# Kernel optimization log

Measured on AMD Instinct MI355X. Metric: run time of the kernel, lower is better.

Reference implementation:

```python
import jax, jax.numpy as jnp
import numpy as np

B, T, D = 2, 2048, 1024
H = 16
DH = D // H


def setup_inputs() -> dict:
    key = jax.random.key(0)
    ks = jax.random.split(key, 6)
    s = 1.0 / np.sqrt(D)
    return {
        "x": jax.random.normal(ks[0], (B, T, D), dtype=jnp.float32),
        "Wq": jax.random.normal(ks[1], (D, D), dtype=jnp.float32) * s,
        "Wk": jax.random.normal(ks[2], (D, D), dtype=jnp.float32) * s,
        "Wv": jax.random.normal(ks[3], (D, D), dtype=jnp.float32) * s,
        "Wo": jax.random.normal(ks[4], (D, D), dtype=jnp.float32) * s,
        "bo": jax.random.normal(ks[5], (D,), dtype=jnp.float32) * s,
    }


def reference(x, Wq, Wk, Wv, Wo, bo):
    b, t, _ = x.shape
    # separate Q/K/V projections (nn.Linear: x @ W.T, no bias)
    q = (x @ Wq.T).reshape(b, t, H, DH).transpose(0, 2, 1, 3)  # [b,h,t,hd]
    k = (x @ Wk.T).reshape(b, t, H, DH).transpose(0, 2, 1, 3)
    v = (x @ Wv.T).reshape(b, t, H, DH).transpose(0, 2, 1, 3)

    scores = jnp.einsum("bhqd,bhkd->bhqk", q, k)  # [b,h,t,t]
    causal = jnp.triu(jnp.ones((t, t), dtype=bool), k=1)
    scores = jnp.where(causal, -jnp.inf, scores)
    weights = jax.nn.softmax(scores / np.sqrt(DH), axis=-1)
    # dropout p=0.0 -> identity
    ctx = jnp.einsum("bhqk,bhkd->bhqd", weights, v)  # [b,h,t,hd]
    # NOTE: original code reshapes WITHOUT transposing heads back — replicate faithfully
    ctx = ctx.reshape(b, t, H * DH)
    return ctx @ Wo.T + bo
```

## Files before the change

### kernel.cpp

```cpp
#include <hip/hip_runtime.h>
#include <math.h>

#define BATCH 2
#define SEQ   2048
#define DIM   1024
#define NH    16
#define HD    64
#define MTOT  4096

typedef __attribute__((ext_vector_type(8)))  short bf16x8;
typedef __attribute__((ext_vector_type(4)))  float f32x4;
typedef __attribute__((ext_vector_type(16))) float f32x16;
typedef __attribute__((ext_vector_type(2)))  float f32x2;
typedef __attribute__((ext_vector_type(2)))  unsigned u32x2;

__device__ __forceinline__ ushort f2bf(float f) {
    union { float f; unsigned u; } v; v.f = f;
    unsigned r = v.u + 0x7fffu + ((v.u >> 16) & 1u);
    return (ushort)(r >> 16);
}

__device__ __forceinline__ unsigned cvtpk_bf16(float lo, float hi) {
    unsigned r;
    asm("v_cvt_pk_bf16_f32 %0, %1, %2" : "=v"(r) : "v"(lo), "v"(hi));
    return r;
}

__device__ __forceinline__ f32x2 pk_add(f32x2 a, f32x2 b) {
    f32x2 d;
    asm("v_pk_add_f32 %0, %1, %2" : "=v"(d) : "v"(a), "v"(b));
    return d;
}

__device__ __forceinline__ f32x2 pk_mul(f32x2 a, f32x2 b) {
    f32x2 d;
    asm("v_pk_mul_f32 %0, %1, %2" : "=v"(d) : "v"(a), "v"(b));
    return d;
}

__device__ __forceinline__ float fmax3(float a, float b, float c) {
    return fmaxf(fmaxf(a, b), c);
}

__global__ __launch_bounds__(256)
void cast_all(const float* __restrict__ x,
              const float* __restrict__ Wq, const float* __restrict__ Wk,
              const float* __restrict__ Wv, const float* __restrict__ Wo,
              ushort* __restrict__ xb,
              ushort* __restrict__ wqb, ushort* __restrict__ wkb,
              ushort* __restrict__ wvb, ushort* __restrict__ wob)
{
    const int z = blockIdx.y;
    const float* s; ushort* d; int n4;
    if (z == 0)      { s = x;  d = xb;  n4 = MTOT * DIM / 4; }
    else if (z == 1) { s = Wq; d = wqb; n4 = DIM * DIM / 4; }
    else if (z == 2) { s = Wk; d = wkb; n4 = DIM * DIM / 4; }
    else if (z == 3) { s = Wv; d = wvb; n4 = DIM * DIM / 4; }
    else             { s = Wo; d = wob; n4 = DIM * DIM / 4; }
    for (int i = blockIdx.x * blockDim.x + threadIdx.x; i < n4;
         i += gridDim.x * blockDim.x) {
        float4 v = ((const float4*)s)[i];
        ushort4 o;
        o.x = f2bf(v.x); o.y = f2bf(v.y); o.z = f2bf(v.z); o.w = f2bf(v.w);
        ((ushort4*)d)[i] = o;
    }
}

template<int MODE>
__global__ __launch_bounds__(256)
void gemm_bf16(const ushort* __restrict__ A,
               const ushort* __restrict__ W0, const ushort* __restrict__ W1,
               const ushort* __restrict__ W2,
               ushort* __restrict__ D0, ushort* __restrict__ D1,
               ushort* __restrict__ D2,
               const float* __restrict__ bias, float* __restrict__ Fout)
{
    __shared__ __align__(16) ushort As[2][128 * 64];
    __shared__ __align__(16) ushort Bs[2][128 * 64];

    const int tid = threadIdx.x;
    const int w = tid >> 6, l = tid & 63;
    const int g = l >> 4, l15 = l & 15;
    const int wr = w >> 1, wc = w & 1;
    const int brow = blockIdx.x * 128, bcol = blockIdx.y * 128;

    const ushort* W = (MODE == 1) ? W0
                    : (blockIdx.z == 0 ? W0 : (blockIdx.z == 1 ? W1 : W2));
    ushort* Dst = (MODE == 1) ? (ushort*)0
                : (blockIdx.z == 0 ? D0 : (blockIdx.z == 1 ? D1 : D2));

    const int rsub = l >> 3;
    const int gc   = ((l & 7) ^ rsub) * 8;
    const size_t arow0 = (size_t)(brow + 32 * w + rsub) * DIM;
    const size_t brow0 = (size_t)(bcol + 32 * w + rsub) * DIM;

    auto STAGE = [&](int buf, int ktel) {
        #pragma unroll
        for (int i = 0; i < 4; ++i) {
            __builtin_amdgcn_global_load_lds(
                (const __attribute__((address_space(1))) void*)
                    &A[arow0 + (size_t)(8 * i) * DIM + ktel + gc],
                (__attribute__((address_space(3))) void*)
                    &As[buf][(32 * w + 8 * i) * 64], 16, 0, 0);
            __builtin_amdgcn_global_load_lds(
                (const __attribute__((address_space(1))) void*)
                    &W[brow0 + (size_t)(8 * i) * DIM + ktel + gc],
                (__attribute__((address_space(3))) void*)
                    &Bs[buf][(32 * w + 8 * i) * 64], 16, 0, 0);
        }
    };

    STAGE(0, 0);
    STAGE(1, 64);

    f32x4 acc[4][4] = {};

    for (int t = 0; t < 16; ++t) {
        const int cur = t & 1;
        if (t < 15) asm volatile("s_waitcnt vmcnt(8)" ::: "memory");
        else        asm volatile("s_waitcnt vmcnt(0)" ::: "memory");
        __builtin_amdgcn_s_barrier();
        __builtin_amdgcn_sched_barrier(0);

        #pragma unroll
        for (int kh = 0; kh < 2; ++kh) {
            bf16x8 af[4], bfr[4];
            #pragma unroll
            for (int mi = 0; mi < 4; ++mi) {
                int row = 64 * wr + 16 * mi + l15;
                af[mi] = *(const bf16x8*)&As[cur][row * 64 + (((4 * kh + g) ^ (row & 7)) * 8)];
            }
            #pragma unroll
            for (int nj = 0; nj < 4; ++nj) {
                int row = 64 * wc + 16 * nj + l15;
                bfr[nj] = *(const bf16x8*)&Bs[cur][row * 64 + (((4 * kh + g) ^ (row & 7)) * 8)];
            }
            __builtin_amdgcn_s_setprio(1);
            #pragma unroll
            for (int mi = 0; mi < 4; ++mi)
                #pragma unroll
                for (int nj = 0; nj < 4; ++nj)
                    acc[mi][nj] = __builtin_amdgcn_mfma_f32_16x16x32_bf16(
                        af[mi], bfr[nj], acc[mi][nj], 0, 0, 0);
            __builtin_amdgcn_s_setprio(0);
        }

        __builtin_amdgcn_sched_barrier(0);
        __builtin_amdgcn_s_barrier();
        if (t + 2 < 16) STAGE(cur, (t + 2) * 64);
    }

    if (MODE == 0) {
        ushort* LB = (ushort*)As;
        const int bB = brow >> 11, t0 = brow & (SEQ - 1);
        if (blockIdx.z == 2) {
            #pragma unroll
            for (int mi = 0; mi < 4; ++mi)
                #pragma unroll
                for (int nj = 0; nj < 4; ++nj) {
                    int tlb = 64 * wr + 16 * mi + 4 * g;
                    int hd = 16 * nj + l15;
                    int sI = (tlb >> 3) * 2 + wc;
                    uint2 pk;
                    pk.x = cvtpk_bf16(acc[mi][nj][0], acc[mi][nj][1]);
                    pk.y = cvtpk_bf16(acc[mi][nj][2], acc[mi][nj][3]);
                    *(uint2*)&LB[sI * 512 + hd * 8 + (tlb & 7)] = pk;
                }
            __syncthreads();
            #pragma unroll
            for (int j = 0; j < 8; ++j) {
                int4 v = *(const int4*)&LB[(j * 256 + tid) * 8];
                int sI = j * 4 + (tid >> 6);
                size_t base = (size_t)(bB * NH + 2 * blockIdx.y + (sI & 1)) * (SEQ * HD)
                            + (size_t)((t0 >> 3) + (sI >> 1)) * 512 + (tid & 63) * 8;
                *(int4*)&Dst[base] = v;
            }
        } else {
            const float osc = (blockIdx.z == 0) ? 0.125f * 1.44269504f : 1.0f;
            #pragma unroll
            for (int mi = 0; mi < 4; ++mi)
                #pragma unroll
                for (int nj = 0; nj < 4; ++nj)
                    #pragma unroll
                    for (int reg = 0; reg < 4; ++reg) {
                        int tl = 64 * wr + 16 * mi + 4 * g + reg;
                        int hd = 16 * nj + l15;
                        int sI = (tl >> 5) * 2 + wc;
                        LB[sI * 2048 + (hd >> 3) * 256 + (tl & 31) * 8 + (hd & 7)] =
                            f2bf(acc[mi][nj][reg] * osc);
                    }
            __syncthreads();
            #pragma unroll
            for (int j = 0; j < 8; ++j) {
                int4 v = *(const int4*)&LB[(j * 256 + tid) * 8];
                size_t base = (size_t)(bB * NH + 2 * blockIdx.y + (j & 1)) * (SEQ * HD)
                            + (size_t)((t0 >> 5) + (j >> 1)) * 2048 + tid * 8;
                *(int4*)&Dst[base] = v;
            }
        }
    } else {
        #pragma unroll
        for (int nj = 0; nj < 4; ++nj) {
            int col = bcol + 64 * wc + 16 * nj + l15;
            float bv = bias[col];
            #pragma unroll
            for (int mi = 0; mi < 4; ++mi)
                #pragma unroll
                for (int reg = 0; reg < 4; ++reg) {
                    int row = brow + 64 * wr + 16 * mi + 4 * g + reg;
                    Fout[(size_t)row * DIM + col] = acc[mi][nj][reg] + bv;
                }
        }
    }
}

__global__ __launch_bounds__(256, 2)
void attn_mfma9(const ushort* __restrict__ q, const ushort* __restrict__ k,
                const ushort* __restrict__ vt, ushort* __restrict__ ctx)
{
    __shared__ float Olds[4 * 2048];
    __shared__ float Mlds[4][32];
    __shared__ float Llds[4][32];

    const int tid = threadIdx.x;
    const int wq = tid >> 6, l = tid & 63;
    const int l31 = l & 31, h = l >> 5;
    const int bh = blockIdx.x;
    const int qt = 63 - (int)blockIdx.y;
    const int qlo = qt * 32;
    const int nt  = (qt >> 1) + 1;
    const int cnt = (nt + 3) >> 2;
    const int kt0 = wq * cnt;
    const int kt1 = min(nt, kt0 + cnt);

    const ushort* Qg = q  + (size_t)bh * SEQ * HD;
    const ushort* Kg = k  + (size_t)bh * SEQ * HD;
    const ushort* Vg = vt + (size_t)bh * SEQ * HD;

    bf16x8 qf[4];
    #pragma unroll
    for (int s = 0; s < 4; ++s)
        qf[s] = *(const bf16x8*)&Qg[(((size_t)qt * 8 + 2 * s + h) * 32 + l31) * 8];

    f32x16 o[2] = {};
    float m = -3.0e38f, lsum = 0.f;

    if (kt0 < kt1) {
        bf16x8 kfA[8], kfB[8], vfA[8], vfB[8];
        #pragma unroll
        for (int s = 0; s < 4; ++s)
            #pragma unroll
            for (int f = 0; f < 2; ++f)
                kfA[2 * s + f] = *(const bf16x8*)
                    &Kg[(((size_t)(2 * kt0 + f) * 8 + 2 * s + h) * 32 + l31) * 8];
        #pragma unroll
        for (int s4 = 0; s4 < 4; ++s4)
            #pragma unroll
            for (int dt = 0; dt < 2; ++dt)
                vfA[2 * s4 + dt] = *(const bf16x8*)
                    &Vg[(((size_t)(8 * kt0 + 2 * s4 + h)) * 64 + 32 * dt + l31) * 8];

        auto body = [&](bf16x8 (&kc)[8], bf16x8 (&kn)[8],
                        bf16x8 (&vc)[8], bf16x8 (&vn)[8], int kt) {
            const int kvb = 64 * kt;

            f32x16 st[2] = {};
            __builtin_amdgcn_s_setprio(1);
            #pragma unroll
            for (int s = 0; s < 4; ++s)
                #pragma unroll
                for (int f = 0; f < 2; ++f)
                    st[f] = __builtin_amdgcn_mfma_f32_32x32x16_bf16(
                        kc[2 * s + f], qf[s], st[f], 0, 0, 0);
            __builtin_amdgcn_s_setprio(0);

            if (kt + 1 < kt1) {
                #pragma unroll
                for (int s = 0; s < 4; ++s)
                    #pragma unroll
                    for (int f = 0; f < 2; ++f)
                        kn[2 * s + f] = *(const bf16x8*)
                            &Kg[(((size_t)(2 * kt + 2 + f) * 8 + 2 * s + h) * 32 + l31) * 8];
                #pragma unroll
                for (int s4 = 0; s4 < 4; ++s4)
                    #pragma unroll
                    for (int dt = 0; dt < 2; ++dt)
                        vn[2 * s4 + dt] = *(const bf16x8*)
                            &Vg[(((size_t)(8 * kt + 8 + 2 * s4 + h)) * 64 + 32 * dt + l31) * 8];
            }

            const int qg = qlo + l31;
            if (kvb + 63 > qlo) {
                #pragma unroll
                for (int f = 0; f < 2; ++f)
                    #pragma unroll
                    for (int r = 0; r < 16; ++r) {
                        int kvg = kvb + 32 * f + (r & 3) + 8 * (r >> 2) + 4 * h;
                        if (kvg > qg) st[f][r] = -INFINITY;
                    }
            }

            float ca, cb;
            ca = fmax3(st[0][0], st[0][1], st[0][2]);
            cb = fmax3(st[0][3], st[0][4], st[0][5]);
            ca = fmax3(ca, st[0][6], st[0][7]);
            cb = fmax3(cb, st[0][8], st[0][9]);
            ca = fmax3(ca, st[0][10], st[0][11]);
            cb = fmax3(cb, st[0][12], st[0][13]);
            ca = fmax3(ca, st[0][14], st[0][15]);
            float t0 = fmaxf(ca, cb);
            ca = fmax3(st[1][0], st[1][1], st[1][2]);
            cb = fmax3(st[1][3], st[1][4], st[1][5]);
            ca = fmax3(ca, st[1][6], st[1][7]);
            cb = fmax3(cb, st[1][8], st[1][9]);
            ca = fmax3(ca, st[1][10], st[1][11]);
            cb = fmax3(cb, st[1][12], st[1][13]);
            ca = fmax3(ca, st[1][14], st[1][15]);
            float tmax = fmax3(t0, ca, cb);
            {
                union { float f; unsigned u; } tm; tm.f = tmax;
                u32x2 ts = __builtin_amdgcn_permlane32_swap(tm.u, tm.u, false, false);
                union { unsigned u; float f; } to; to.u = h ? ts.x : ts.y;
                tmax = fmaxf(tmax, to.f);
            }

            if (!__all(tmax - m <= 8.0f)) {
                float mn = fmaxf(m, tmax);
                float sc = exp2f(m - mn);
                lsum *= sc;
                f32x2 sc2 = {sc, sc};
                #pragma unroll
                for (int dt = 0; dt < 2; ++dt) {
                    f32x2* po = (f32x2*)&o[dt];
                    #pragma unroll
                    for (int i = 0; i < 8; ++i) po[i] = pk_mul(po[i], sc2);
                }
                m = mn;
            }

            f32x2 mneg = {-m, -m};
            f32x2 a0 = {0.f, 0.f}, a1 = {0.f, 0.f}, a2 = {0.f, 0.f}, a3 = {0.f, 0.f};
            #pragma unroll
            for (int f = 0; f < 2; ++f) {
                f32x2* pp = (f32x2*)&st[f];
                #pragma unroll
                for (int i = 0; i < 8; ++i) {
                    f32x2 t = pk_add(pp[i], mneg);
                    t.x = exp2f(t.x); t.y = exp2f(t.y);
                    pp[i] = t;
                    if ((i & 3) == 0)      a0 = pk_add(a0, t);
                    else if ((i & 3) == 1) a1 = pk_add(a1, t);
                    else if ((i & 3) == 2) a2 = pk_add(a2, t);
                    else                   a3 = pk_add(a3, t);
                }
            }
            a0 = pk_add(a0, a1);
            a2 = pk_add(a2, a3);
            a0 = pk_add(a0, a2);
            lsum += a0.x + a0.y;

            #pragma unroll
            for (int s4 = 0; s4 < 4; ++s4) {
                const int f = s4 >> 1, rb2 = 8 * (s4 & 1);
                unsigned Aa = cvtpk_bf16(st[f][rb2 + 0], st[f][rb2 + 1]);
                unsigned Bb = cvtpk_bf16(st[f][rb2 + 2], st[f][rb2 + 3]);
                unsigned Cc = cvtpk_bf16(st[f][rb2 + 4], st[f][rb2 + 5]);
                unsigned Dd = cvtpk_bf16(st[f][rb2 + 6], st[f][rb2 + 7]);
                u32x2 r02 = __builtin_amdgcn_permlane32_swap(Aa, Cc, false, false);
                u32x2 r13 = __builtin_amdgcn_permlane32_swap(Bb, Dd, false, false);
                union { unsigned wv[4]; bf16x8 v; } pu;
                pu.wv[0] = r02.x;
                pu.wv[1] = r13.x;
                pu.wv[2] = r02.y;
                pu.wv[3] = r13.y;
                __builtin_amdgcn_s_setprio(1);
                #pragma unroll
                for (int dt = 0; dt < 2; ++dt)
                    o[dt] = __builtin_amdgcn_mfma_f32_32x32x16_bf16(
                        vc[2 * s4 + dt], pu.v, o[dt], 0, 0, 0);
                __builtin_amdgcn_s_setprio(0);
            }
        };

        int kt = kt0;
        while (true) {
            body(kfA, kfB, vfA, vfB, kt);
            if (++kt >= kt1) break;
            body(kfB, kfA, vfB, vfA, kt);
            if (++kt >= kt1) break;
        }
    }

    float lt = lsum + __shfl_xor(lsum, 32);
    if (h == 0) Mlds[wq][l31] = m;
    __syncthreads();
    float ms = fmaxf(fmaxf(Mlds[0][l31], Mlds[1][l31]),
                     fmaxf(Mlds[2][l31], Mlds[3][l31]));
    float fw = exp2f(m - ms);
    if (h == 0) Llds[wq][l31] = lt * fw;
    #pragma unroll
    for (int dt = 0; dt < 2; ++dt)
        #pragma unroll
        for (int r = 0; r < 16; ++r) {
            int d = 32 * dt + (r & 3) + 8 * (r >> 2) + 4 * h;
            Olds[wq * 2048 + d * 32 + (l31 ^ (d & 31))] = o[dt][r] * fw;
        }
    __syncthreads();

    const int tq = tid >> 3, tc = tid & 7;
    float inv = 1.0f / (Llds[0][tq] + Llds[1][tq] + Llds[2][tq] + Llds[3][tq]);
    union { ushort u[8]; int4 v4; } ov;
    #pragma unroll
    for (int i = 0; i < 8; i += 2) {
        int d0 = 8 * tc + i, d1 = d0 + 1;
        float s0 = 0.f, s1 = 0.f;
        #pragma unroll
        for (int ww = 0; ww < 4; ++ww) {
            s0 += Olds[ww * 2048 + d0 * 32 + (tq ^ (d0 & 31))];
            s1 += Olds[ww * 2048 + d1 * 32 + (tq ^ (d1 & 31))];
        }
        *(unsigned*)&ov.u[i] = cvtpk_bf16(s0 * inv, s1 * inv);
    }
    ushort* Cg = ctx + (size_t)bh * SEQ * HD + (size_t)qlo * HD;
    *(int4*)&Cg[tq * 64 + 8 * tc] = ov.v4;
}

extern "C" void kernel_launch(void* const* d_in, const int* in_sizes, int n_in,
                              void* d_out, int out_size, void* d_ws, size_t ws_size,
                              hipStream_t stream)
{
    (void)in_sizes; (void)n_in; (void)out_size; (void)ws_size;
    const float* x  = (const float*)d_in[0];
    const float* Wq = (const float*)d_in[1];
    const float* Wk = (const float*)d_in[2];
    const float* Wv = (const float*)d_in[3];
    const float* Wo = (const float*)d_in[4];
    const float* bo = (const float*)d_in[5];
    float* out = (float*)d_out;

    ushort* wsu  = (ushort*)d_ws;
    ushort* xb   = wsu;
    ushort* wqb  = wsu + 4194304;
    ushort* wkb  = wsu + 5242880;
    ushort* wvb  = wsu + 6291456;
    ushort* wob  = wsu + 7340032;
    ushort* qbuf = wsu + 8388608;
    ushort* kbuf = wsu + 12582912;
    ushort* vtb  = wsu + 16777216;
    ushort* ctxb = wsu + 20971520;

    cast_all<<<dim3(512, 5), 256, 0, stream>>>(x, Wq, Wk, Wv, Wo,
                                               xb, wqb, wkb, wvb, wob);

    dim3 gqkv(MTOT / 128, DIM / 128, 3);
    gemm_bf16<0><<<gqkv, 256, 0, stream>>>(xb, wqb, wkb, wvb,
                                           qbuf, kbuf, vtb, nullptr, nullptr);

    dim3 ga(BATCH * NH, SEQ / 32);
    attn_mfma9<<<ga, 256, 0, stream>>>(qbuf, kbuf, vtb, ctxb);

    dim3 go(MTOT / 128, DIM / 128, 1);
    gemm_bf16<1><<<go, 256, 0, stream>>>(ctxb, wob, nullptr, nullptr,
                                         nullptr, nullptr, nullptr, bo, out);
}
```

Baseline: 106.9 us.

## Raise attention occupancy, drop V double-buffering, pack bf16 LDS reduce, coalesce output GEMM stores

Result: slower. 267.2 us (+150.0%).

```diff
diff --git a/kernel.cpp b/kernel.cpp
--- a/kernel.cpp
+++ b/kernel.cpp
@@ -26,6 +26,12 @@
     return r;
 }
 
+__device__ __forceinline__ float exp2_asm(float x) {
+    float r;
+    asm("v_exp_f32 %0, %1" : "=v"(r) : "v"(x));
+    return r;
+}
+
 __device__ __forceinline__ f32x2 pk_add(f32x2 a, f32x2 b) {
     f32x2 d;
     asm("v_pk_add_f32 %0, %1, %2" : "=v"(d) : "v"(a), "v"(b));
@@ -40,6 +46,13 @@
 
 __device__ __forceinline__ float fmax3(float a, float b, float c) {
     return fmaxf(fmaxf(a, b), c);
+}
+
+__device__ __forceinline__ float bf_lo(unsigned u) {
+    union { unsigned u; float f; } v; v.u = u << 16; return v.f;
+}
+__device__ __forceinline__ float bf_hi(unsigned u) {
+    union { unsigned u; float f; } v; v.u = u & 0xffff0000u; return v.f;
 }
 
 __global__ __launch_bounds__(256)
@@ -199,26 +212,40 @@
             }
         }
     } else {
-        #pragma unroll
-        for (int nj = 0; nj < 4; ++nj) {
-            int col = bcol + 64 * wc + 16 * nj + l15;
-            float bv = bias[col];
-            #pragma unroll
-            for (int mi = 0; mi < 4; ++mi)
-                #pragma unroll
-                for (int reg = 0; reg < 4; ++reg) {
-                    int row = brow + 64 * wr + 16 * mi + 4 * g + reg;
-                    Fout[(size_t)row * DIM + col] = acc[mi][nj][reg] + bv;
-                }
+        float* BF = (float*)As;
+        const int trow = tid >> 3, tc8 = tid & 7;
+        float4 bias4[4];
+        #pragma unroll
+        for (int j = 0; j < 4; ++j)
+            bias4[j] = *(const float4*)&bias[bcol + tc8 * 16 + j * 4];
+        #pragma unroll
+        for (int mi = 0; mi < 4; ++mi) {
+            __syncthreads();
+            #pragma unroll
+            for (int nj = 0; nj < 4; ++nj) {
+                int col = 64 * wc + 16 * nj + l15;
+                #pragma unroll
+                for (int reg = 0; reg < 4; ++reg)
+                    BF[(wr * 16 + 4 * g + reg) * 132 + col] = acc[mi][nj][reg];
+            }
+            __syncthreads();
+            int grow = brow + 64 * (trow >> 4) + 16 * mi + (trow & 15);
+            #pragma unroll
+            for (int j = 0; j < 4; ++j) {
+                float4 v = *(const float4*)&BF[trow * 132 + tc8 * 16 + j * 4];
+                v.x += bias4[j].x; v.y += bias4[j].y;
+                v.z += bias4[j].z; v.w += bias4[j].w;
+                *(float4*)&Fout[(size_t)grow * DIM + bcol + tc8 * 16 + j * 4] = v;
+            }
         }
     }
 }
 
-__global__ __launch_bounds__(256, 2)
-void attn_mfma9(const ushort* __restrict__ q, const ushort* __restrict__ k,
-                const ushort* __restrict__ vt, ushort* __restrict__ ctx)
+__global__ __launch_bounds__(256, 5)
+void attn_mfma13(const ushort* __restrict__ q, const ushort* __restrict__ k,
+                 const ushort* __restrict__ vt, ushort* __restrict__ ctx)
 {
-    __shared__ float Olds[4 * 2048];
+    __shared__ unsigned OldsU[4 * 1024];
     __shared__ float Mlds[4][32];
     __shared__ float Llds[4][32];
 
@@ -246,23 +273,30 @@
     float m = -3.0e38f, lsum = 0.f;
 
     if (kt0 < kt1) {
-        bf16x8 kfA[8], kfB[8], vfA[8], vfB[8];
+        bf16x8 kfA[8], kfB[8];
+
         #pragma unroll
         for (int s = 0; s < 4; ++s)
             #pragma unroll
             for (int f = 0; f < 2; ++f)
                 kfA[2 * s + f] = *(const bf16x8*)
                     &Kg[(((size_t)(2 * kt0 + f) * 8 + 2 * s + h) * 32 + l31) * 8];
-        #pragma unroll
-        for (int s4 = 0; s4 < 4; ++s4)
-            #pragma unroll
-            for (int dt = 0; dt < 2; ++dt)
-                vfA[2 * s4 + dt] = *(const bf16x8*)
-                    &Vg[(((size_t)(8 * kt0 + 2 * s4 + h)) * 64 + 32 * dt + l31) * 8];
-
-        auto body = [&](bf16x8 (&kc)[8], bf16x8 (&kn)[8],
-                        bf16x8 (&vc)[8], bf16x8 (&vn)[8], int kt) {
+
+        const ushort* kpa = Kg + (((size_t)(16 * (kt0 + 1)) + h) * 32 + l31) * 8;
+        const ushort* kpb = kpa + 2048;
+        const ushort* vpa = Vg + (((size_t)(8 * kt0) + h) * 64 + l31) * 8;
+        const ushort* vpb = vpa + 2048;
+
+        auto body = [&](bf16x8 (&kc)[8], bf16x8 (&kn)[8], int kt) {
             const int kvb = 64 * kt;
+
+            bf16x8 vf[8];
+            #pragma unroll
+            for (int s4 = 0; s4 < 4; ++s4)
+                #pragma unroll
+                for (int dt = 0; dt < 2; ++dt)
+                    vf[2 * s4 + dt] = *(const bf16x8*)
+                        ((s4 < 2 ? vpa : vpb) + (s4 & 1) * 1024 + dt * 256);
 
             f32x16 st[2] = {};
             __builtin_amdgcn_s_setprio(1);
@@ -280,13 +314,7 @@
                     #pragma unroll
                     for (int f = 0; f < 2; ++f)
                         kn[2 * s + f] = *(const bf16x8*)
-                            &Kg[(((size_t)(2 * kt + 2 + f) * 8 + 2 * s + h) * 32 + l31) * 8];
-                #pragma unroll
-                for (int s4 = 0; s4 < 4; ++s4)
-                    #pragma unroll
-                    for (int dt = 0; dt < 2; ++dt)
-                        vn[2 * s4 + dt] = *(const bf16x8*)
-                            &Vg[(((size_t)(8 * kt + 8 + 2 * s4 + h)) * 64 + 32 * dt + l31) * 8];
+                            ((f ? kpb : kpa) + s * 512);
             }
 
             const int qg = qlo + l31;
@@ -326,7 +354,7 @@
 
             if (!__all(tmax - m <= 8.0f)) {
                 float mn = fmaxf(m, tmax);
-                float sc = exp2f(m - mn);
+                float sc = exp2_asm(m - mn);
                 lsum *= sc;
                 f32x2 sc2 = {sc, sc};
                 #pragma unroll
@@ -346,7 +374,7 @@
                 #pragma unroll
                 for (int i = 0; i < 8; ++i) {
                     f32x2 t = pk_add(pp[i], mneg);
-                    t.x = exp2f(t.x); t.y = exp2f(t.y);
+                    t.x = exp2_asm(t.x); t.y = exp2_asm(t.y);
                     pp[i] = t;
                     if ((i & 3) == 0)      a0 = pk_add(a0, t);
                     else if ((i & 3) == 1) a1 = pk_add(a1, t);
@@ -377,16 +405,19 @@
                 #pragma unroll
                 for (int dt = 0; dt < 2; ++dt)
                     o[dt] = __builtin_amdgcn_mfma_f32_32x32x16_bf16(
-                        vc[2 * s4 + dt], pu.v, o[dt], 0, 0, 0);
+                        vf[2 * s4 + dt], pu.v, o[dt], 0, 0, 0);
                 __builtin_amdgcn_s_setprio(0);
             }
+
+            kpa += 4096; kpb += 4096;
+            vpa += 4096; vpb += 4096;
         };
 
         int kt = kt0;
         while (true) {
-            body(kfA, kfB, vfA, vfB, kt);
+            body(kfA, kfB, kt);
             if (++kt >= kt1) break;
-            body(kfB, kfA, vfB, vfA, kt);
+            body(kfB, kfA, kt);
             if (++kt >= kt1) break;
         }
     }
@@ -396,14 +427,15 @@
     __syncthreads();
     float ms = fmaxf(fmaxf(Mlds[0][l31], Mlds[1][l31]),
                      fmaxf(Mlds[2][l31], Mlds[3][l31]));
-    float fw = exp2f(m - ms);
+    float fw = exp2_asm(m - ms);
     if (h == 0) Llds[wq][l31] = lt * fw;
     #pragma unroll
     for (int dt = 0; dt < 2; ++dt)
         #pragma unroll
-        for (int r = 0; r < 16; ++r) {
-            int d = 32 * dt + (r & 3) + 8 * (r >> 2) + 4 * h;
-            Olds[wq * 2048 + d * 32 + (l31 ^ (d & 31))] = o[dt][r] * fw;
+        for (int r = 0; r < 16; r += 2) {
+            int du = 16 * dt + ((r & 3) >> 1) + 4 * (r >> 2) + 2 * h;
+            OldsU[wq * 1024 + l31 * 32 + (du ^ l31)] =
+                cvtpk_bf16(o[dt][r] * fw, o[dt][r + 1] * fw);
         }
     __syncthreads();
 
@@ -412,12 +444,12 @@
     union { ushort u[8]; int4 v4; } ov;
     #pragma unroll
     for (int i = 0; i < 8; i += 2) {
-        int d0 = 8 * tc + i, d1 = d0 + 1;
+        int du = 4 * tc + (i >> 1);
         float s0 = 0.f, s1 = 0.f;
         #pragma unroll
         for (int ww = 0; ww < 4; ++ww) {
-            s0 += Olds[ww * 2048 + d0 * 32 + (tq ^ (d0 & 31))];
-            s1 += Olds[ww * 2048 + d1 * 32 + (tq ^ (d1 & 31))];
+            unsigned v = OldsU[ww * 1024 + tq * 32 + (du ^ tq)];
+            s0 += bf_lo(v); s1 += bf_hi(v);
         }
         *(unsigned*)&ov.u[i] = cvtpk_bf16(s0 * inv, s1 * inv);
     }
@@ -457,7 +489,7 @@
                                            qbuf, kbuf, vtb, nullptr, nullptr);
 
     dim3 ga(BATCH * NH, SEQ / 32);
-    attn_mfma9<<<ga, 256, 0, stream>>>(qbuf, kbuf, vtb, ctxb);
+    attn_mfma13<<<ga, 256, 0, stream>>>(qbuf, kbuf, vtb, ctxb);
 
     dim3 go(MTOT / 128, DIM / 128, 1);
     gemm_bf16<1><<<go, 256, 0, stream>>>(ctxb, wob, nullptr, nullptr,
```
